# Optimization experiments

Hardware: AMD Instinct MI355X
Metric: run time of the kernel (lower is better)

The kernel has to match this reference:

```python
import jax, jax.numpy as jnp
import numpy as np

NUM_HEADS = 16

def setup_inputs() -> dict:
    key = jax.random.key(0)
    k1, k2, k3 = jax.random.split(key, 3)
    T, B, E = 2048, 4, 1024
    x = jax.random.normal(k1, (T, B, E), dtype=jnp.float32)
    # xavier-ish scale for weights
    in_proj_w = jax.random.normal(k2, (3 * E, E), dtype=jnp.float32) * (1.0 / np.sqrt(E))
    in_proj_b = jnp.zeros((3 * E,), dtype=jnp.float32)
    out_w = jax.random.normal(k3, (E, E), dtype=jnp.float32) * (1.0 / np.sqrt(E))
    out_b = jnp.zeros((E,), dtype=jnp.float32)
    return {"x": x, "in_proj_w": in_proj_w, "in_proj_b": in_proj_b, "out_w": out_w, "out_b": out_b}

def reference(x, in_proj_w, in_proj_b, out_w, out_b):
    # Self-attention (qkv_same path), dropout=0, eval mode, no masks.
    T, B, E = x.shape
    H = NUM_HEADS
    Dh = E // H
    scaling = Dh ** (-0.5)
    # fused in-projection: [T,B,3E]
    qkv = jnp.einsum('tbe,fe->tbf', x, in_proj_w) + in_proj_b
    q, k, v = jnp.split(qkv, 3, axis=-1)
    q = q * scaling
    # [T,B,E] -> [B,H,T,Dh]
    def to_heads(t):
        return t.reshape(T, B, H, Dh).transpose(1, 2, 0, 3)
    q, k, v = to_heads(q), to_heads(k), to_heads(v)
    # full TxT score matrix, softmax in float32 (matches F.softmax(..., dtype=float32))
    scores = jnp.einsum('bhtd,bhsd->bhts', q, k)
    attn_weights = jax.nn.softmax(scores.astype(jnp.float32), axis=-1).astype(scores.dtype)
    attn = jnp.einsum('bhts,bhsd->bhtd', attn_weights, v)
    # [B,H,T,Dh] -> [T,B,E]
    attn = attn.transpose(2, 0, 1, 3).reshape(T, B, E)
    attn = jnp.einsum('tbe,fe->tbf', attn, out_w) + out_b
    # need_weights=True: average over heads -> [B,T,T]
    avg_weights = attn_weights.sum(axis=1) / H
    return attn, avg_weights
```

## Files before the change

kernel.cpp:

```cpp
#include <hip/hip_runtime.h>
#include <stdint.h>

#define DEV __device__ __forceinline__

typedef __attribute__((ext_vector_type(8))) __bf16 bf16x8;
typedef __attribute__((ext_vector_type(4))) __bf16 bf16x4;
typedef __attribute__((ext_vector_type(4))) float f32x4;

DEV unsigned short f2bf(float f){
  union { float fv; unsigned u; } v; v.fv = f;
  unsigned r = v.u + 0x7fffu + ((v.u >> 16) & 1u);
  return (unsigned short)(r >> 16);
}

DEV void gload16(const void* g, void* l){
  __builtin_amdgcn_global_load_lds((const __attribute__((address_space(1))) void*)g,
                                   (__attribute__((address_space(3))) void*)l,
                                   16, 0, 0);
}

__global__ void k_cvt(const float* __restrict__ src, unsigned short* __restrict__ dst){
  const int i = (blockIdx.x * blockDim.x + threadIdx.x) << 2;
  const float4 v = *(const float4*)(src + i);
  ushort4 o;
  o.x = f2bf(v.x); o.y = f2bf(v.y); o.z = f2bf(v.z); o.w = f2bf(v.w);
  *(ushort4*)(dst + i) = o;
}

template<int MODE>
__launch_bounds__(512, 4)
__global__ void k_gemm(const unsigned short* __restrict__ A,
                       const unsigned short* __restrict__ Bm,
                       const float* __restrict__ bias,
                       float* __restrict__ outF,
                       unsigned short* __restrict__ Qm,
                       unsigned short* __restrict__ Km,
                       unsigned short* __restrict__ VTm)
{
  __shared__ unsigned short As[2][128*64];
  __shared__ unsigned short Bs[2][128*64];
  const int tid  = threadIdx.x;
  const int lane = tid & 63;
  const int wid  = tid >> 6;
  const int wr   = wid >> 1;
  const int wc   = wid & 1;
  const int l15  = lane & 15;
  const int l4   = lane >> 4;
  const int wg  = blockIdx.x;
  const int by  = (wg & 7)*8 + ((wg >> 3) & 7);
  const int bx  = wg >> 6;
  const int r0  = by * 128;
  const int c0  = bx * 128;

  f32x4 acc[2][4];
#pragma unroll
  for (int m = 0; m < 2; ++m)
#pragma unroll
    for (int n = 0; n < 4; ++n)
      acc[m][n] = (f32x4){0.f, 0.f, 0.f, 0.f};

  auto STAGE = [&](int buf, int kt){
    const int k0 = kt << 6;
#pragma unroll
    for (int i = 0; i < 2; ++i){
      const int s = i*512 + tid;
      const int row = s >> 3;
      const int cg = (s & 7) ^ (row & 7);
      gload16(A + (size_t)(r0 + row)*1024 + k0 + cg*8, (void*)(&As[buf][s*8]));
    }
#pragma unroll
    for (int i = 0; i < 2; ++i){
      const int s = i*512 + tid;
      const int row = s >> 3;
      const int cg = (s & 7) ^ (row & 7);
      gload16(Bm + (size_t)(c0 + row)*1024 + k0 + cg*8, (void*)(&Bs[buf][s*8]));
    }
  };

  auto COMPUTE = [&](int buf){
#pragma unroll
    for (int kk = 0; kk < 2; ++kk){
      bf16x8 af[2], bf[4];
#pragma unroll
      for (int m = 0; m < 2; ++m){
        const int row = wr*32 + m*16 + l15;
        const int ch  = (kk*4 + l4) ^ (row & 7);
        af[m] = *(const bf16x8*)(&As[buf][row*64 + ch*8]);
      }
#pragma unroll
      for (int n = 0; n < 4; ++n){
        const int row = wc*64 + n*16 + l15;
        const int ch  = (kk*4 + l4) ^ (row & 7);
        bf[n] = *(const bf16x8*)(&Bs[buf][row*64 + ch*8]);
      }
      __builtin_amdgcn_s_setprio(1);
#pragma unroll
      for (int m = 0; m < 2; ++m)
#pragma unroll
        for (int n = 0; n < 4; ++n)
          acc[m][n] = __builtin_amdgcn_mfma_f32_16x16x32_bf16(af[m], bf[n], acc[m][n], 0, 0, 0);
      __builtin_amdgcn_s_setprio(0);
    }
  };

  STAGE(0, 0);
  for (int t = 0; t < 15; ++t){
    const int cur = t & 1;
    STAGE(cur ^ 1, t + 1);
    asm volatile("s_waitcnt vmcnt(4)" ::: "memory");
    asm volatile("s_barrier" ::: "memory");
    COMPUTE(cur);
    asm volatile("s_waitcnt lgkmcnt(0)" ::: "memory");
    asm volatile("s_barrier" ::: "memory");
  }
  asm volatile("s_waitcnt vmcnt(0)" ::: "memory");
  asm volatile("s_barrier" ::: "memory");
  COMPUTE(1);

  if (MODE == 0){
#pragma unroll
    for (int n = 0; n < 4; ++n){
      const int f     = c0 + wc*64 + n*16 + l15;
      const float bs  = bias[f];
      const int which = f >> 10;
      const int fi    = f & 1023;
      const int h     = fi >> 6;
      const int d     = fi & 63;
#pragma unroll
      for (int m = 0; m < 2; ++m){
        const int rb = r0 + wr*32 + m*16 + (l4 << 2);
#pragma unroll
        for (int j = 0; j < 4; ++j){
          const int r = rb + j;
          const int t = r >> 2;
          const int b = r & 3;
          float v = acc[m][n][j] + bs;
          if (which == 0) v *= 0.18033688f;
          const unsigned short bv = f2bf(v);
          const int bh = b*16 + h;
          if (which == 0)      Qm [((size_t)bh*2048 + t)*64 + d] = bv;
          else if (which == 1) Km [((size_t)bh*2048 + t)*64 + d] = bv;
          else                 VTm[((size_t)bh*64 + d)*2048 + t] = bv;
        }
      }
    }
  } else {
#pragma unroll
    for (int m = 0; m < 2; ++m){
      const int rb = r0 + wr*32 + m*16 + (l4 << 2);
#pragma unroll
      for (int n = 0; n < 4; ++n){
        const int f    = c0 + wc*64 + n*16 + l15;
        const float bs = bias[f];
#pragma unroll
        for (int j = 0; j < 4; ++j)
          outF[(size_t)(rb + j)*1024 + f] = acc[m][n][j] + bs;
      }
    }
  }
}

__launch_bounds__(512)
__global__ void k_pv(const unsigned short* __restrict__ Qm,
                     const unsigned short* __restrict__ Km,
                     const unsigned short* __restrict__ VTm,
                     float* __restrict__ linv,
                     unsigned short* __restrict__ ctx)
{
  __shared__ unsigned short Ws[256*64];
  __shared__ unsigned short Ks[2][64*64];
  __shared__ unsigned short Vs[2][64*64];
  const int tid = threadIdx.x, lane = tid & 63, wid = tid >> 6;
  const int l15 = lane & 15, l4 = lane >> 4;
  const int wg = blockIdx.x;
  const int slot = wg >> 3;
  const int bh = (wg & 7)*8 + (slot >> 3);
  const int t0 = (slot & 7) * 256;
  const unsigned short* Qb = Qm  + (size_t)bh*131072;
  const unsigned short* Kb = Km  + (size_t)bh*131072;
  const unsigned short* Vb = VTm + (size_t)bh*131072;

  {
    const int s = tid;
    const int row = s >> 3;
    const int cg = (s & 7) ^ (row & 7);
    gload16(Kb + (size_t)row*64 + cg*8, (void*)(Ks[0] + s*8));
    gload16(Vb + (size_t)row*2048 + cg*8, (void*)(Vs[0] + s*8));
  }
  bf16x8 aq[2][2];
#pragma unroll
  for (int qs = 0; qs < 2; ++qs)
#pragma unroll
    for (int kk = 0; kk < 2; ++kk)
      aq[qs][kk] = *(const bf16x8*)(Qb + (size_t)(t0 + wid*32 + qs*16 + l15)*64 + (kk*4 + l4)*8);
  __syncthreads();

  f32x4 oacc[2][4];
#pragma unroll
  for (int qs = 0; qs < 2; ++qs)
#pragma unroll
    for (int n = 0; n < 4; ++n) oacc[qs][n] = (f32x4){0.f,0.f,0.f,0.f};
  float lacc[2] = {0.f, 0.f};
  const int rx = l15 & 7;

  for (int s0 = 0; s0 < 2048; s0 += 64){
    const int cur = (s0 >> 6) & 1;
    if (s0 + 64 < 2048){
      const int s = tid;
      const int row = s >> 3;
      const int cg = (s & 7) ^ (row & 7);
      gload16(Kb + (size_t)(s0 + 64 + row)*64 + cg*8, (void*)(Ks[cur^1] + s*8));
      gload16(Vb + (size_t)row*2048 + (s0 + 64) + cg*8, (void*)(Vs[cur^1] + s*8));
    }
#pragma unroll
    for (int n = 0; n < 4; ++n){
      bf16x8 ak[2];
#pragma unroll
      for (int kk = 0; kk < 2; ++kk){
        const int ch = (kk*4 + l4) ^ rx;
        ak[kk] = *(const bf16x8*)(Ks[cur] + (n*16 + l15)*64 + ch*8);
      }
#pragma unroll
      for (int qs = 0; qs < 2; ++qs){
        f32x4 sacc = (f32x4){0.f,0.f,0.f,0.f};
        sacc = __builtin_amdgcn_mfma_f32_16x16x32_bf16(ak[0], aq[qs][0], sacc, 0, 0, 0);
        sacc = __builtin_amdgcn_mfma_f32_16x16x32_bf16(ak[1], aq[qs][1], sacc, 0, 0, 0);
        f32x4 pv;
        pv[0] = __builtin_amdgcn_exp2f(sacc[0]);
        pv[1] = __builtin_amdgcn_exp2f(sacc[1]);
        pv[2] = __builtin_amdgcn_exp2f(sacc[2]);
        pv[3] = __builtin_amdgcn_exp2f(sacc[3]);
        lacc[qs] += (pv[0] + pv[1]) + (pv[2] + pv[3]);
        const bf16x4 pb = __builtin_convertvector(pv, bf16x4);
        const int wrow = wid*32 + qs*16 + l15;
        const int g = (n*4 + l4) ^ (rx << 1);
        *(bf16x4*)(Ws + wrow*64 + g*4) = pb;
      }
    }
    bf16x8 aw[2][2];
#pragma unroll
    for (int qs = 0; qs < 2; ++qs)
#pragma unroll
      for (int kk = 0; kk < 2; ++kk){
        const int c = (kk*4 + l4) ^ rx;
        aw[qs][kk] = *(const bf16x8*)(Ws + (wid*32 + qs*16 + l15)*64 + c*8);
      }
#pragma unroll
    for (int n = 0; n < 4; ++n){
#pragma unroll
      for (int kk = 0; kk < 2; ++kk){
        const int ch = (kk*4 + l4) ^ rx;
        const bf16x8 bv = *(const bf16x8*)(Vs[cur] + (n*16 + l15)*64 + ch*8);
#pragma unroll
        for (int qs = 0; qs < 2; ++qs)
          oacc[qs][n] = __builtin_amdgcn_mfma_f32_16x16x32_bf16(aw[qs][kk], bv, oacc[qs][n], 0, 0, 0);
      }
    }
    __syncthreads();
  }

  const int b = bh >> 4, h = bh & 15;
#pragma unroll
  for (int qs = 0; qs < 2; ++qs){
    lacc[qs] += __shfl_xor(lacc[qs], 16);
    lacc[qs] += __shfl_xor(lacc[qs], 32);
    const float rl = 1.0f / lacc[qs];
    if (lane < 16)
      linv[(size_t)bh*2048 + t0 + wid*32 + qs*16 + lane] = rl;
    float rlj[4];
#pragma unroll
    for (int j = 0; j < 4; ++j)
      rlj[j] = __shfl(rl, (l4 << 2) + j);
#pragma unroll
    for (int n = 0; n < 4; ++n){
#pragma unroll
      for (int j = 0; j < 4; ++j){
        const int t = t0 + wid*32 + qs*16 + (l4 << 2) + j;
        const int d = n*16 + l15;
        ctx[((size_t)t*4 + b)*1024 + h*64 + d] = f2bf(oacc[qs][n][j] * rlj[j]);
      }
    }
  }
}

__launch_bounds__(256)
__global__ void k_avg(const unsigned short* __restrict__ Qm,
                      const unsigned short* __restrict__ Km,
                      const float* __restrict__ linv,
                      float* __restrict__ avg)
{
  __shared__ unsigned short Ks[2][128*64];
  const int tid = threadIdx.x, lane = tid & 63, wid = tid >> 6;
  const int l15 = lane & 15, l4 = lane >> 4;
  const int wg = blockIdx.x;
  const int slot = wg >> 3;
  const int combo = (wg & 7) + 8*(slot >> 4);
  const int b   = combo >> 4;
  const int s0  = (combo & 15) * 128;
  const int t0  = (slot & 15) * 128;
  const int rx  = l15 & 7;

  float wacc[2][8][4];
#pragma unroll
  for (int qs = 0; qs < 2; ++qs)
#pragma unroll
    for (int n = 0; n < 8; ++n)
#pragma unroll
      for (int j = 0; j < 4; ++j) wacc[qs][n][j] = 0.f;

  {
    const unsigned short* Kb = Km + (size_t)(b*16)*131072;
#pragma unroll
    for (int i = 0; i < 4; ++i){
      const int s = i*256 + tid;
      const int row = s >> 3;
      const int cg = (s & 7) ^ (row & 7);
      gload16(Kb + (size_t)(s0 + row)*64 + cg*8, (void*)(Ks[0] + s*8));
    }
  }

  for (int h = 0; h < 16; ++h){
    const int cur = h & 1;
    const int bh = b*16 + h;
    const unsigned short* Qb = Qm + (size_t)bh*131072;

    bf16x8 aq[2][2];
#pragma unroll
    for (int qs = 0; qs < 2; ++qs)
#pragma unroll
      for (int kk = 0; kk < 2; ++kk)
        aq[qs][kk] = *(const bf16x8*)(Qb + (size_t)(t0 + wid*32 + qs*16 + l15)*64 + (kk*4 + l4)*8);

    float4 lj[2];
#pragma unroll
    for (int qs = 0; qs < 2; ++qs){
      lj[qs] = *(const float4*)(linv + (size_t)bh*2048 + t0 + wid*32 + qs*16 + (l4 << 2));
      lj[qs].x *= 0.0625f; lj[qs].y *= 0.0625f; lj[qs].z *= 0.0625f; lj[qs].w *= 0.0625f;
    }

    if (h < 15){
      const unsigned short* Kb = Km + (size_t)(b*16 + h + 1)*131072;
#pragma unroll
      for (int i = 0; i < 4; ++i){
        const int s = i*256 + tid;
        const int row = s >> 3;
        const int cg = (s & 7) ^ (row & 7);
        gload16(Kb + (size_t)(s0 + row)*64 + cg*8, (void*)(Ks[cur^1] + s*8));
      }
      asm volatile("s_waitcnt vmcnt(4)" ::: "memory");
    } else {
      asm volatile("s_waitcnt vmcnt(0)" ::: "memory");
    }
    asm volatile("s_barrier" ::: "memory");

#pragma unroll
    for (int n = 0; n < 8; ++n){
      bf16x8 bk[2];
#pragma unroll
      for (int kk = 0; kk < 2; ++kk){
        const int ch = (kk*4 + l4) ^ rx;
        bk[kk] = *(const bf16x8*)(Ks[cur] + (n*16 + l15)*64 + ch*8);
      }
#pragma unroll
      for (int qs = 0; qs < 2; ++qs){
        f32x4 sacc = (f32x4){0.f,0.f,0.f,0.f};
        sacc = __builtin_amdgcn_mfma_f32_16x16x32_bf16(aq[qs][0], bk[0], sacc, 0, 0, 0);
        sacc = __builtin_amdgcn_mfma_f32_16x16x32_bf16(aq[qs][1], bk[1], sacc, 0, 0, 0);
        wacc[qs][n][0] += __builtin_amdgcn_exp2f(sacc[0]) * lj[qs].x;
        wacc[qs][n][1] += __builtin_amdgcn_exp2f(sacc[1]) * lj[qs].y;
        wacc[qs][n][2] += __builtin_amdgcn_exp2f(sacc[2]) * lj[qs].z;
        wacc[qs][n][3] += __builtin_amdgcn_exp2f(sacc[3]) * lj[qs].w;
      }
    }
    asm volatile("s_waitcnt lgkmcnt(0)" ::: "memory");
    asm volatile("s_barrier" ::: "memory");
  }

#pragma unroll
  for (int qs = 0; qs < 2; ++qs)
#pragma unroll
    for (int n = 0; n < 8; ++n)
#pragma unroll
      for (int j = 0; j < 4; ++j){
        const int t = t0 + wid*32 + qs*16 + (l4 << 2) + j;
        const int s = s0 + n*16 + l15;
        avg[((size_t)b*2048 + t)*2048 + s] = wacc[qs][n][j];
      }
}

extern "C" void kernel_launch(void* const* d_in, const int* in_sizes, int n_in,
                              void* d_out, int out_size, void* d_ws, size_t ws_size,
                              hipStream_t stream)
{
  const float* x    = (const float*)d_in[0];
  const float* wqkv = (const float*)d_in[1];
  const float* bqkv = (const float*)d_in[2];
  const float* wout = (const float*)d_in[3];
  const float* bout = (const float*)d_in[4];
  float* out = (float*)d_out;

  char* ws = (char*)d_ws;
  unsigned short* xb    = (unsigned short*)(ws);
  unsigned short* wqkvb = (unsigned short*)(ws + ((size_t)16 << 20));
  unsigned short* woutb = (unsigned short*)(ws + ((size_t)24 << 20));
  unsigned short* Qm    = (unsigned short*)(ws + ((size_t)26 << 20));
  unsigned short* Km    = (unsigned short*)(ws + ((size_t)42 << 20));
  unsigned short* VTm   = (unsigned short*)(ws + ((size_t)58 << 20));
  unsigned short* ctx   = (unsigned short*)(ws + ((size_t)74 << 20));
  float* linv = (float*)(ws + ((size_t)90 << 20));

  k_cvt<<<8192, 256, 0, stream>>>(x,    xb);
  k_cvt<<<3072, 256, 0, stream>>>(wqkv, wqkvb);
  k_cvt<<<1024, 256, 0, stream>>>(wout, woutb);

  k_gemm<0><<<1536, 512, 0, stream>>>(xb, wqkvb, bqkv, nullptr, Qm, Km, VTm);
  k_pv     <<< 512, 512, 0, stream>>>(Qm, Km, VTm, linv, ctx);
  k_avg    <<<1024, 256, 0, stream>>>(Qm, Km, linv, out + 8388608);
  k_gemm<1><<< 512, 512, 0, stream>>>(ctx, woutb, bout, out, nullptr, nullptr, nullptr);
}
```

Baseline: 262.9 us.

## Feed softmax probabilities to PV MFMA from registers, dropping LDS staging

The P·V step now consumes the bf16 probability fragments straight from the QK^T MFMA output registers, using the 16x16x16 bf16 MFMA whose operand layout matches. This removes the shared-memory write and read-back of the weight tile and the Ws buffer. Workgroups shrink to 256 threads covering 128 query rows and the grid doubles to 1024, with each thread issuing two K/V prefetch loads. s_setprio is raised around the MFMAs. The trade-off is smaller-K MFMAs, more of them, and more blocks that each reload the full K/V stream.

```diff
diff --git a/kernel.cpp b/kernel.cpp
--- a/kernel.cpp
+++ b/kernel.cpp
@@ -6,6 +6,7 @@
 typedef __attribute__((ext_vector_type(8))) __bf16 bf16x8;
 typedef __attribute__((ext_vector_type(4))) __bf16 bf16x4;
 typedef __attribute__((ext_vector_type(4))) float f32x4;
+typedef __attribute__((ext_vector_type(4))) short short4v;
 
 DEV unsigned short f2bf(float f){
   union { float fv; unsigned u; } v; v.fv = f;
@@ -160,28 +161,28 @@
   }
 }
 
-__launch_bounds__(512)
+__launch_bounds__(256)
 __global__ void k_pv(const unsigned short* __restrict__ Qm,
                      const unsigned short* __restrict__ Km,
                      const unsigned short* __restrict__ VTm,
                      float* __restrict__ linv,
                      unsigned short* __restrict__ ctx)
 {
-  __shared__ unsigned short Ws[256*64];
   __shared__ unsigned short Ks[2][64*64];
   __shared__ unsigned short Vs[2][64*64];
   const int tid = threadIdx.x, lane = tid & 63, wid = tid >> 6;
   const int l15 = lane & 15, l4 = lane >> 4;
   const int wg = blockIdx.x;
   const int slot = wg >> 3;
-  const int bh = (wg & 7)*8 + (slot >> 3);
-  const int t0 = (slot & 7) * 256;
+  const int bh = (wg & 7)*8 + (slot >> 4);
+  const int t0 = (slot & 15) * 128;
   const unsigned short* Qb = Qm  + (size_t)bh*131072;
   const unsigned short* Kb = Km  + (size_t)bh*131072;
   const unsigned short* Vb = VTm + (size_t)bh*131072;
 
-  {
-    const int s = tid;
+#pragma unroll
+  for (int i = 0; i < 2; ++i){
+    const int s = i*256 + tid;
     const int row = s >> 3;
     const int cg = (s & 7) ^ (row & 7);
     gload16(Kb + (size_t)row*64 + cg*8, (void*)(Ks[0] + s*8));
@@ -199,18 +200,21 @@
 #pragma unroll
   for (int qs = 0; qs < 2; ++qs)
 #pragma unroll
-    for (int n = 0; n < 4; ++n) oacc[qs][n] = (f32x4){0.f,0.f,0.f,0.f};
+    for (int d = 0; d < 4; ++d) oacc[qs][d] = (f32x4){0.f,0.f,0.f,0.f};
   float lacc[2] = {0.f, 0.f};
   const int rx = l15 & 7;
 
   for (int s0 = 0; s0 < 2048; s0 += 64){
     const int cur = (s0 >> 6) & 1;
     if (s0 + 64 < 2048){
-      const int s = tid;
-      const int row = s >> 3;
-      const int cg = (s & 7) ^ (row & 7);
-      gload16(Kb + (size_t)(s0 + 64 + row)*64 + cg*8, (void*)(Ks[cur^1] + s*8));
-      gload16(Vb + (size_t)row*2048 + (s0 + 64) + cg*8, (void*)(Vs[cur^1] + s*8));
+#pragma unroll
+      for (int i = 0; i < 2; ++i){
+        const int s = i*256 + tid;
+        const int row = s >> 3;
+        const int cg = (s & 7) ^ (row & 7);
+        gload16(Kb + (size_t)(s0 + 64 + row)*64 + cg*8, (void*)(Ks[cur^1] + s*8));
+        gload16(Vb + (size_t)row*2048 + (s0 + 64) + cg*8, (void*)(Vs[cur^1] + s*8));
+      }
     }
 #pragma unroll
     for (int n = 0; n < 4; ++n){
@@ -220,40 +224,33 @@
         const int ch = (kk*4 + l4) ^ rx;
         ak[kk] = *(const bf16x8*)(Ks[cur] + (n*16 + l15)*64 + ch*8);
       }
+      short4v pb[2];
 #pragma unroll
       for (int qs = 0; qs < 2; ++qs){
         f32x4 sacc = (f32x4){0.f,0.f,0.f,0.f};
+        __builtin_amdgcn_s_setprio(1);
         sacc = __builtin_amdgcn_mfma_f32_16x16x32_bf16(ak[0], aq[qs][0], sacc, 0, 0, 0);
         sacc = __builtin_amdgcn_mfma_f32_16x16x32_bf16(ak[1], aq[qs][1], sacc, 0, 0, 0);
+        __builtin_amdgcn_s_setprio(0);
         f32x4 pv;
         pv[0] = __builtin_amdgcn_exp2f(sacc[0]);
         pv[1] = __builtin_amdgcn_exp2f(sacc[1]);
         pv[2] = __builtin_amdgcn_exp2f(sacc[2]);
         pv[3] = __builtin_amdgcn_exp2f(sacc[3]);
         lacc[qs] += (pv[0] + pv[1]) + (pv[2] + pv[3]);
-        const bf16x4 pb = __builtin_convertvector(pv, bf16x4);
-        const int wrow = wid*32 + qs*16 + l15;
-        const int g = (n*4 + l4) ^ (rx << 1);
-        *(bf16x4*)(Ws + wrow*64 + g*4) = pb;
-      }
-    }
-    bf16x8 aw[2][2];
-#pragma unroll
-    for (int qs = 0; qs < 2; ++qs)
-#pragma unroll
-      for (int kk = 0; kk < 2; ++kk){
-        const int c = (kk*4 + l4) ^ rx;
-        aw[qs][kk] = *(const bf16x8*)(Ws + (wid*32 + qs*16 + l15)*64 + c*8);
-      }
-#pragma unroll
-    for (int n = 0; n < 4; ++n){
-#pragma unroll
-      for (int kk = 0; kk < 2; ++kk){
-        const int ch = (kk*4 + l4) ^ rx;
-        const bf16x8 bv = *(const bf16x8*)(Vs[cur] + (n*16 + l15)*64 + ch*8);
+        bf16x4 pbf = __builtin_convertvector(pv, bf16x4);
+        pb[qs] = *(short4v*)&pbf;
+      }
+#pragma unroll
+      for (int d = 0; d < 4; ++d){
+        const int drow = d*16 + l15;
+        const int ch   = (n*2 + (l4 >> 1)) ^ rx;
+        const short4v bv = *(const short4v*)(Vs[cur] + drow*64 + ch*8 + (l4 & 1)*4);
+        __builtin_amdgcn_s_setprio(1);
 #pragma unroll
         for (int qs = 0; qs < 2; ++qs)
-          oacc[qs][n] = __builtin_amdgcn_mfma_f32_16x16x32_bf16(aw[qs][kk], bv, oacc[qs][n], 0, 0, 0);
+          oacc[qs][d] = __builtin_amdgcn_mfma_f32_16x16x16bf16_1k(pb[qs], bv, oacc[qs][d], 0, 0, 0);
+        __builtin_amdgcn_s_setprio(0);
       }
     }
     __syncthreads();
@@ -272,12 +269,12 @@
     for (int j = 0; j < 4; ++j)
       rlj[j] = __shfl(rl, (l4 << 2) + j);
 #pragma unroll
-    for (int n = 0; n < 4; ++n){
+    for (int d = 0; d < 4; ++d){
 #pragma unroll
       for (int j = 0; j < 4; ++j){
         const int t = t0 + wid*32 + qs*16 + (l4 << 2) + j;
-        const int d = n*16 + l15;
-        ctx[((size_t)t*4 + b)*1024 + h*64 + d] = f2bf(oacc[qs][n][j] * rlj[j]);
+        const int dd = d*16 + l15;
+        ctx[((size_t)t*4 + b)*1024 + h*64 + dd] = f2bf(oacc[qs][d][j] * rlj[j]);
       }
     }
   }
@@ -414,7 +411,7 @@
   k_cvt<<<1024, 256, 0, stream>>>(wout, woutb);
 
   k_gemm<0><<<1536, 512, 0, stream>>>(xb, wqkvb, bqkv, nullptr, Qm, Km, VTm);
-  k_pv     <<< 512, 512, 0, stream>>>(Qm, Km, VTm, linv, ctx);
+  k_pv     <<<1024, 256, 0, stream>>>(Qm, Km, VTm, linv, ctx);
   k_avg    <<<1024, 256, 0, stream>>>(Qm, Km, linv, out + 8388608);
   k_gemm<1><<< 512, 512, 0, stream>>>(ctx, woutb, bout, out, nullptr, nullptr, nullptr);
 }
```

After: 283.9 us. 1.08x slower.
